# Optimization experiments

Measured on AMD Instinct MI355X. Metric: run time of the kernel, lower is better.

The kernel has to match this reference:

```python
import jax, jax.numpy as jnp
import numpy as np

D_MODEL = 1024
N_HEADS = 16
WINDOW = 64              # window_size
HEAD_DIM = D_MODEL // N_HEADS
HALF = WINDOW // 2
NWIN = WINDOW + 1        # half tokens each side + self
LN_EPS = 1e-5


def _layernorm(x, g, b):
    mu = jnp.mean(x, axis=-1, keepdims=True)
    var = jnp.var(x, axis=-1, keepdims=True)
    return (x - mu) * jax.lax.rsqrt(var + LN_EPS) * g + b


def _linear_attention(q, k, v):
    # feature map phi(x) = elu(x) + 1; O(n) attention over full d_model
    q = jax.nn.elu(q) + 1.0
    k = jax.nn.elu(k) + 1.0
    kv = jnp.einsum('bsd,bse->bde', k, v)          # [B, D, D]
    num = jnp.einsum('bsd,bde->bse', q, kv)        # [B, S, D]
    denom = jnp.einsum('bsd,bd->bs', q, k.sum(axis=1))
    return num / (denom[..., None] + 1e-6)


def _window_attention(q, k, v, rel_bias):
    # sliding window attention with relative position bias, banded via offset scan
    B, S, _ = q.shape
    qh = q.reshape(B, S, N_HEADS, HEAD_DIM).transpose(0, 2, 1, 3)  # [B,H,S,Dh]
    kh = k.reshape(B, S, N_HEADS, HEAD_DIM).transpose(0, 2, 1, 3)
    vh = v.reshape(B, S, N_HEADS, HEAD_DIM).transpose(0, 2, 1, 3)
    kp = jnp.pad(kh, ((0, 0), (0, 0), (HALF, HALF), (0, 0)))
    vp = jnp.pad(vh, ((0, 0), (0, 0), (HALF, HALF), (0, 0)))
    pos = jnp.arange(S)
    scale = np.float32(1.0 / np.sqrt(HEAD_DIM))

    def score_step(_, w):
        off = w - HALF                                   # relative offset in [-HALF, HALF]
        ks = jax.lax.dynamic_slice_in_dim(kp, w, S, axis=2)   # k at position i+off
        s = jnp.einsum('bhsd,bhsd->bhs', qh, ks) * scale
        s = s + rel_bias[off + WINDOW][None, :, None]    # bias per head for this offset
        valid = (pos + off >= 0) & (pos + off < S)
        s = jnp.where(valid[None, None, :], s, -jnp.inf)
        return None, s

    _, scores = jax.lax.scan(score_step, None, jnp.arange(NWIN))  # [W,B,H,S]
    attn = jax.nn.softmax(scores, axis=0)                          # softmax over window

    def out_step(acc, aw):
        a, w = aw
        vs = jax.lax.dynamic_slice_in_dim(vp, w, S, axis=2)
        return acc + a[..., None] * vs, None

    out, _ = jax.lax.scan(out_step, jnp.zeros_like(qh), (attn, jnp.arange(NWIN)))
    return out.transpose(0, 2, 1, 3).reshape(B, S, D_MODEL)


def setup_inputs() -> dict:
    key = jax.random.key(0)
    ks = jax.random.split(key, 16)

    def lin(k, fan_in, shape):
        return (jax.random.normal(k, shape, jnp.float32) / np.sqrt(fan_in)).astype(jnp.float32)

    D = D_MODEL
    inp = {
        'x': jax.random.normal(ks[0], (2, 2048, D), jnp.float32),
        'wq_lin': lin(ks[1], D, (D, D)), 'bq_lin': jnp.zeros((D,), jnp.float32),
        'wk_lin': lin(ks[2], D, (D, D)), 'bk_lin': jnp.zeros((D,), jnp.float32),
        'wv_lin': lin(ks[3], D, (D, D)), 'bv_lin': jnp.zeros((D,), jnp.float32),
        'wq_loc': lin(ks[4], D, (D, D)), 'bq_loc': jnp.zeros((D,), jnp.float32),
        'wk_loc': lin(ks[5], D, (D, D)), 'bk_loc': jnp.zeros((D,), jnp.float32),
        'wv_loc': lin(ks[6], D, (D, D)), 'bv_loc': jnp.zeros((D,), jnp.float32),
        'wo': lin(ks[7], D, (D, D)), 'bo': jnp.zeros((D,), jnp.float32),
        'wg1': lin(ks[8], 3 * D, (3 * D, D)), 'bg1': jnp.zeros((D,), jnp.float32),
        'wg2': lin(ks[9], D, (D, D)), 'bg2': jnp.zeros((D,), jnp.float32),
        'rel_bias': jax.random.normal(ks[10], (2 * WINDOW + 1, N_HEADS), jnp.float32),
        'ln_g': jnp.ones((D,), jnp.float32),
        'ln_b': jnp.zeros((D,), jnp.float32),
    }
    return inp


def reference(x, wq_lin, bq_lin, wk_lin, bk_lin, wv_lin, bv_lin,
              wq_loc, bq_loc, wk_loc, bk_loc, wv_loc, bv_loc,
              wo, bo, wg1, bg1, wg2, bg2, rel_bias, ln_g, ln_b):
    h = _layernorm(x, ln_g, ln_b)
    lin_out = _linear_attention(h @ wq_lin + bq_lin,
                                h @ wk_lin + bk_lin,
                                h @ wv_lin + bv_lin)
    win_out = _window_attention(h @ wq_loc + bq_loc,
                                h @ wk_loc + bk_loc,
                                h @ wv_loc + bv_loc, rel_bias)
    gate_in = jnp.concatenate([lin_out, win_out, h], axis=-1)
    gate = jax.nn.sigmoid(jnp.maximum(gate_in @ wg1 + bg1, 0.0) @ wg2 + bg2)
    out = gate * lin_out + (1.0 - gate) * win_out
    return out @ wo + bo + x
```

## Files before the change

kernel.cpp:

```cpp
#include <hip/hip_runtime.h>

typedef unsigned short u16;
typedef unsigned int u32;
typedef float f32x4 __attribute__((ext_vector_type(4)));
typedef __bf16 bf16x8 __attribute__((ext_vector_type(8)));

#define SEQ 2048
#define DM 1024

__device__ __forceinline__ float bf2f(u16 a){
  u32 b = ((u32)a) << 16; float f; __builtin_memcpy(&f, &b, 4); return f;
}
__device__ __forceinline__ u16 f2bf(float f){
  u32 b; __builtin_memcpy(&b, &f, 4);
  b += 0x7fffu + ((b >> 16) & 1u);
  return (u16)(b >> 16);
}

__device__ __forceinline__ void gload16(const void* g, void* l){
  __builtin_amdgcn_global_load_lds((const __attribute__((address_space(1))) u32*)g,
                                   (__attribute__((address_space(3))) u32*)l, 16, 0, 0);
}

#define SBAR  __builtin_amdgcn_sched_barrier(0); __builtin_amdgcn_s_barrier(); __builtin_amdgcn_sched_barrier(0);
#define VM0   asm volatile("s_waitcnt vmcnt(0)" ::: "memory"); __builtin_amdgcn_sched_barrier(0);
#define VM6   asm volatile("s_waitcnt vmcnt(6)" ::: "memory"); __builtin_amdgcn_sched_barrier(0);
#define VM8   asm volatile("s_waitcnt vmcnt(8)" ::: "memory"); __builtin_amdgcn_sched_barrier(0);

#define MFMA16(AF, BF) \
  __builtin_amdgcn_s_setprio(1); \
  _Pragma("unroll") for (int m_ = 0; m_ < 4; m_++) \
  _Pragma("unroll") for (int n_ = 0; n_ < 4; n_++) \
    acc[m_][n_] = __builtin_amdgcn_mfma_f32_16x16x32_bf16(AF[m_], BF[n_], acc[m_][n_], 0,0,0); \
  __builtin_amdgcn_s_setprio(0);

struct TP { const float* src[9]; u16* dst[9]; int K[9]; };

__global__ __launch_bounds__(256) void ktransall(TP tp){
  __shared__ float tile[64][65];
  int z = blockIdx.z;
  int K = tp.K[z];
  int kb = blockIdx.y << 6, nb = blockIdx.x << 6;
  if (kb >= K) return;
  const float* W = tp.src[z];
  u16* WT = tp.dst[z];
  const int N = 1024;
  int t = threadIdx.x;
  #pragma unroll
  for (int i = 0; i < 4; i++){
    int idx = t + (i << 8);
    int r = idx >> 4, c = (idx & 15) << 2;
    float4 v = *(const float4*)(W + (size_t)(kb + r) * N + nb + c);
    tile[r][c] = v.x; tile[r][c+1] = v.y; tile[r][c+2] = v.z; tile[r][c+3] = v.w;
  }
  __syncthreads();
  #pragma unroll
  for (int i = 0; i < 2; i++){
    int idx = t + (i << 8);
    int n = idx >> 3, k8 = (idx & 7) << 3;
    union { u16 s[8]; int4 v; } u;
    #pragma unroll
    for (int j = 0; j < 8; j++) u.s[j] = f2bf(tile[k8 + j][n]);
    *(int4*)(WT + (size_t)(nb + n) * K + kb + k8) = u.v;
  }
}

__global__ __launch_bounds__(256) void kln(const float* __restrict__ x, const float* __restrict__ gg,
                                           const float* __restrict__ bb, u16* __restrict__ h){
  int row = blockIdx.x, t = threadIdx.x;
  float4 xv = ((const float4*)(x + (size_t)row * DM))[t];
  float s  = xv.x + xv.y + xv.z + xv.w;
  float s2 = xv.x*xv.x + xv.y*xv.y + xv.z*xv.z + xv.w*xv.w;
  #pragma unroll
  for (int o = 1; o < 64; o <<= 1){ s += __shfl_xor(s, o); s2 += __shfl_xor(s2, o); }
  __shared__ float r1[4], r2[4];
  if ((t & 63) == 0){ r1[t >> 6] = s; r2[t >> 6] = s2; }
  __syncthreads();
  float S = r1[0]+r1[1]+r1[2]+r1[3], S2 = r2[0]+r2[1]+r2[2]+r2[3];
  float mu = S * (1.0f/DM);
  float var = S2 * (1.0f/DM) - mu*mu;
  float rstd = rsqrtf(var + 1e-5f);
  float4 gv = ((const float4*)gg)[t], bv = ((const float4*)bb)[t];
  ushort4 o;
  o.x = f2bf((xv.x - mu)*rstd*gv.x + bv.x);
  o.y = f2bf((xv.y - mu)*rstd*gv.y + bv.y);
  o.z = f2bf((xv.z - mu)*rstd*gv.z + bv.z);
  o.w = f2bf((xv.w - mu)*rstd*gv.w + bv.w);
  ((ushort4*)(h + (size_t)row * DM))[t] = o;
}

__device__ __forceinline__ float phi_elu(float v){ return v > 0.f ? v + 1.f : __expf(v); }

__global__ __launch_bounds__(512, 2) void kqkv8(
  const u16* __restrict__ h,
  const u16* wt0, const u16* wt1, const u16* wt2, const u16* wt3, const u16* wt4, const u16* wt5,
  const float* b0, const float* b1, const float* b2, const float* b3, const float* b4, const float* b5,
  u16* phiQ, u16* phiKT, u16* vT, u16* qloc, u16* kloc, u16* vlocT)
{
  extern __shared__ char smem[];
  char* LA0 = smem;
  char* LA1 = smem + 16384;
  char* LB0 = smem + 32768;
  char* LB1 = smem + 65536;

  const int t = threadIdx.x, lane = t & 63, w = t >> 6;
  const int wm = w >> 2, wn = w & 3;

  int bid = blockIdx.x;
  int swz = (bid & 7) * 96 + (bid >> 3);
  int mt = swz & 31, ntile = swz >> 5;
  int m0 = mt << 7;
  int n0g = ntile << 8;
  int wi = n0g >> 10;
  int n0 = n0g & 1023;
  const u16* Bp = wi==0?wt0: wi==1?wt1: wi==2?wt2: wi==3?wt3: wi==4?wt4: wt5;
  const float* bsel = wi==0?b0: wi==1?b1: wi==2?b2: wi==3?b3: wi==4?b4: b5;

  auto stageA = [&](char* dst, int kt){
    #pragma unroll
    for (int j = 0; j < 2; j++){
      int slot = (j << 9) + t;
      int r = slot >> 3;
      int csw = ((slot & 7) << 4) ^ ((r & 7) << 4);
      gload16((const char*)(h + (size_t)(m0 + r) * 1024 + (kt << 6)) + csw,
              dst + (((j << 9) + (w << 6)) << 4));
    }
  };
  auto stageB = [&](char* dst, int kt){
    #pragma unroll
    for (int j = 0; j < 4; j++){
      int slot = (j << 9) + t;
      int r = slot >> 3;
      int csw = ((slot & 7) << 4) ^ ((r & 7) << 4);
      gload16((const char*)(Bp + (size_t)(n0 + r) * 1024 + (kt << 6)) + csw,
              dst + (((j << 9) + (w << 6)) << 4));
    }
  };
  auto rdA = [&](const char* ab, int m, int kk) -> bf16x8 {
    int ra = (wm << 6) + (m << 4) + (lane & 15);
    return *(const bf16x8*)(ab + (ra << 7) + (((kk << 6) + ((lane >> 4) << 4)) ^ ((ra & 7) << 4)));
  };
  auto rdB = [&](const char* bb, int n, int kk) -> bf16x8 {
    int rb = (wn << 6) + (n << 4) + (lane & 15);
    return *(const bf16x8*)(bb + (rb << 7) + (((kk << 6) + ((lane >> 4) << 4)) ^ ((rb & 7) << 4)));
  };

  f32x4 acc[4][4];
  #pragma unroll
  for (int m = 0; m < 4; m++)
    #pragma unroll
    for (int n = 0; n < 4; n++) acc[m][n] = (f32x4){0.f,0.f,0.f,0.f};

  const int NT = 16;
  bf16x8 a0[4], bq0[4], a1[4], bq1[4];

  stageA(LA0, 0); stageB(LB0, 0);
  stageA(LA1, 1); stageB(LB1, 1);
  VM6 SBAR
  #pragma unroll
  for (int m = 0; m < 4; m++) a0[m] = rdA(LA0, m, 0);
  #pragma unroll
  for (int n = 0; n < 4; n++) bq0[n] = rdB(LB0, n, 0);

  #pragma unroll 1
  for (int i = 0; i < NT/2; i++){
    int e = 2*i, o = e + 1;
    int se = (e + 2 < NT) ? e + 2 : NT - 1;
    int so = (o + 2 < NT) ? o + 2 : NT - 1;
    #pragma unroll
    for (int m = 0; m < 4; m++) a1[m] = rdA(LA0, m, 1);
    #pragma unroll
    for (int n = 0; n < 4; n++) bq1[n] = rdB(LB0, n, 1);
    SBAR
    stageA(LA0, se); stageB(LB0, se);
    MFMA16(a0, bq0)
    VM6 SBAR
    #pragma unroll
    for (int m = 0; m < 4; m++) a0[m] = rdA(LA1, m, 0);
    #pragma unroll
    for (int n = 0; n < 4; n++) bq0[n] = rdB(LB1, n, 0);
    MFMA16(a1, bq1)
    #pragma unroll
    for (int m = 0; m < 4; m++) a1[m] = rdA(LA1, m, 1);
    #pragma unroll
    for (int n = 0; n < 4; n++) bq1[n] = rdB(LB1, n, 1);
    SBAR
    stageA(LA1, so); stageB(LB1, so);
    MFMA16(a0, bq0)
    VM6 SBAR
    if (i < NT/2 - 1){
      #pragma unroll
      for (int m = 0; m < 4; m++) a0[m] = rdA(LA0, m, 0);
      #pragma unroll
      for (int n = 0; n < 4; n++) bq0[n] = rdB(LB0, n, 0);
    }
    MFMA16(a1, bq1)
  }
  VM0

  #pragma unroll
  for (int n = 0; n < 4; n++){
    int col = n0 + (wn << 6) + (n << 4) + (lane & 15);
    float bv = bsel[col];
    #pragma unroll
    for (int m = 0; m < 4; m++){
      int r0 = m0 + (wm << 6) + (m << 4) + ((lane >> 4) << 2);
      float e[4];
      #pragma unroll
      for (int r = 0; r < 4; r++) e[r] = acc[m][n][r] + bv;
      if (wi == 0){
        #pragma unroll
        for (int r = 0; r < 4; r++) phiQ[(size_t)(r0 + r) * DM + col] = f2bf(phi_elu(e[r]));
      } else if (wi == 1 || wi == 2 || wi == 5){
        union { u16 s[4]; ushort4 v; } o;
        #pragma unroll
        for (int r = 0; r < 4; r++) o.s[r] = f2bf(wi == 1 ? phi_elu(e[r]) : e[r]);
        int bb = r0 >> 11, sl = r0 & 2047;
        u16* dst = (wi == 1) ? phiKT : (wi == 2 ? vT : vlocT);
        *(ushort4*)(dst + ((size_t)(bb << 10) + col) * SEQ + sl) = o.v;
      } else {
        u16* dst = wi==3 ? qloc : kloc;
        #pragma unroll
        for (int r = 0; r < 4; r++) dst[(size_t)(r0 + r) * DM + col] = f2bf(e[r]);
      }
    }
  }
}

template<int NCHUNK>
__device__ __forceinline__ void pipe128(const u16* A0c, const u16* A1c, const u16* A2c, int lda,
                                        const u16* B, int ldb, int K, int m0, int n0,
                                        char* LA0, char* LA1, char* LB0, char* LB1,
                                        f32x4 (&acc)[4][4])
{
  const int t = threadIdx.x, lane = t & 63, w = t >> 6;
  const int wm = w >> 1, wn = w & 1;
  const int NT = K >> 6;

  auto stageA = [&](char* dst, int kt){
    const u16* Ab;
    if (NCHUNK == 3){
      int ci = kt >> 4;
      const u16* cp = (ci == 0) ? A0c : ((ci == 1) ? A1c : A2c);
      Ab = cp + ((kt & 15) << 6);
    } else {
      Ab = A0c + (kt << 6);
    }
    #pragma unroll
    for (int j = 0; j < 4; j++){
      int slot = (j << 8) + t;
      int r = slot >> 3;
      int csw = ((slot & 7) << 4) ^ ((r & 7) << 4);
      gload16((const char*)(Ab + (size_t)(m0 + r) * lda) + csw,
              dst + (((j << 8) + (w << 6)) << 4));
    }
  };
  auto stageB = [&](char* dst, int kt){
    const u16* Bb = B + (kt << 6);
    #pragma unroll
    for (int j = 0; j < 4; j++){
      int slot = (j << 8) + t;
      int r = slot >> 3;
      int csw = ((slot & 7) << 4) ^ ((r & 7) << 4);
      gload16((const char*)(Bb + (size_t)(n0 + r) * ldb) + csw,
              dst + (((j << 8) + (w << 6)) << 4));
    }
  };
  auto rdA = [&](const char* ab, int m, int kk) -> bf16x8 {
    int ra = (wm << 6) + (m << 4) + (lane & 15);
    return *(const bf16x8*)(ab + (ra << 7) + (((kk << 6) + ((lane >> 4) << 4)) ^ ((ra & 7) << 4)));
  };
  auto rdB = [&](const char* bb, int n, int kk) -> bf16x8 {
    int rb = (wn << 6) + (n << 4) + (lane & 15);
    return *(const bf16x8*)(bb + (rb << 7) + (((kk << 6) + ((lane >> 4) << 4)) ^ ((rb & 7) << 4)));
  };

  bf16x8 a0[4], bq0[4], a1[4], bq1[4];

  stageA(LA0, 0); stageB(LB0, 0);
  stageA(LA1, 1); stageB(LB1, 1);
  VM8 SBAR
  #pragma unroll
  for (int m = 0; m < 4; m++) a0[m] = rdA(LA0, m, 0);
  #pragma unroll
  for (int n = 0; n < 4; n++) bq0[n] = rdB(LB0, n, 0);

  #pragma unroll 1
  for (int i = 0; i < NT/2; i++){
    int e = 2*i, o = e + 1;
    int se = (e + 2 < NT) ? e + 2 : NT - 1;
    int so = (o + 2 < NT) ? o + 2 : NT - 1;
    #pragma unroll
    for (int m = 0; m < 4; m++) a1[m] = rdA(LA0, m, 1);
    #pragma unroll
    for (int n = 0; n < 4; n++) bq1[n] = rdB(LB0, n, 1);
    SBAR
    stageA(LA0, se); stageB(LB0, se);
    MFMA16(a0, bq0)
    VM8 SBAR
    #pragma unroll
    for (int m = 0; m < 4; m++) a0[m] = rdA(LA1, m, 0);
    #pragma unroll
    for (int n = 0; n < 4; n++) bq0[n] = rdB(LB1, n, 0);
    MFMA16(a1, bq1)
    #pragma unroll
    for (int m = 0; m < 4; m++) a1[m] = rdA(LA1, m, 1);
    #pragma unroll
    for (int n = 0; n < 4; n++) bq1[n] = rdB(LB1, n, 1);
    SBAR
    stageA(LA1, so); stageB(LB1, so);
    MFMA16(a0, bq0)
    VM8 SBAR
    if (i < NT/2 - 1){
      #pragma unroll
      for (int m = 0; m < 4; m++) a0[m] = rdA(LA0, m, 0);
      #pragma unroll
      for (int n = 0; n < 4; n++) bq0[n] = rdB(LB0, n, 0);
    }
    MFMA16(a1, bq1)
  }
  VM0
}

#define PIPE_LDS \
  __shared__ char LA0[16384], LA1[16384], LB0[16384], LB1[16384];

#define EPI_COORDS \
  const int lane = threadIdx.x & 63, w = threadIdx.x >> 6; \
  const int wm = w >> 1, wn = w & 1;

#define ZERO_ACC f32x4 acc[4][4]; \
  _Pragma("unroll") for (int m = 0; m < 4; m++) _Pragma("unroll") for (int n = 0; n < 4; n++) acc[m][n] = (f32x4){0.f,0.f,0.f,0.f};

__global__ __launch_bounds__(256) void kkv2(const u16* __restrict__ vT, const u16* __restrict__ phiKT,
                                            u16* __restrict__ kvp0, u16* __restrict__ kvp1){
  PIPE_LDS
  int bid = blockIdx.x;
  int mt = bid & 7, nt = (bid >> 3) & 7, b = (bid >> 6) & 1, kh = bid >> 7;
  int m0 = mt << 7, n0 = nt << 7;
  const u16* A = vT + (size_t)b * DM * SEQ + (kh << 10);
  const u16* B = phiKT + (size_t)b * DM * SEQ + (kh << 10);
  ZERO_ACC
  pipe128<1>(A, 0, 0, SEQ, B, SEQ, 1024, m0, n0, LA0, LA1, LB0, LB1, acc);
  EPI_COORDS
  u16* C = (kh ? kvp1 : kvp0) + (size_t)b * DM * DM;
  #pragma unroll
  for (int n = 0; n < 4; n++){
    int col = n0 + wn*64 + n*16 + (lane & 15);
    #pragma unroll
    for (int m = 0; m < 4; m++){
      int r0 = m0 + wm*64 + m*16 + ((lane >> 4) << 2);
      #pragma unroll
      for (int r = 0; r < 4; r++) C[(size_t)(r0 + r) * DM + col] = f2bf(acc[m][n][r]);
    }
  }
}

__global__ __launch_bounds__(256) void kvadd(const u16* __restrict__ a, const u16* __restrict__ bsrc,
                                             u16* __restrict__ c){
  size_t i = ((size_t)blockIdx.x * 256 + threadIdx.x) * 8;
  int4 ra = *(const int4*)(a + i);
  int4 rb = *(const int4*)(bsrc + i);
  const u16* pa = (const u16*)&ra; const u16* pb = (const u16*)&rb;
  union { u16 s[8]; int4 v; } o;
  #pragma unroll
  for (int j = 0; j < 8; j++) o.s[j] = f2bf(bf2f(pa[j]) + bf2f(pb[j]));
  *(int4*)(c + i) = o.v;
}

__global__ __launch_bounds__(256) void kwinM(
  const u16* __restrict__ qloc, const u16* __restrict__ kloc,
  const u16* __restrict__ vlocT, const float* __restrict__ rel_bias,
  u16* __restrict__ wout)
{
  __shared__ char Qs[8192];
  __shared__ char Ks[16384];
  __shared__ char Vs[16384];
  __shared__ char Ps[16384];
  __shared__ float bias_s[65];

  const int t = threadIdx.x, lane = t & 63, w = t >> 6;
  int bid = blockIdx.x;
  int qt = bid & 31, hh = (bid >> 5) & 15, b = bid >> 9;
  int q0 = qt << 6;
  size_t rowbase = (size_t)b * SEQ;

  #pragma unroll
  for (int j = 0; j < 2; j++){
    int c = (j << 8) + t;
    int row = c >> 3;
    int csw = ((c & 7) << 4) ^ ((row & 7) << 4);
    gload16((const char*)(qloc + (rowbase + q0 + row) * DM + hh*64) + csw,
            Qs + (((j << 8) + (w << 6)) << 4));
  }
  #pragma unroll
  for (int j = 0; j < 4; j++){
    int c = (j << 8) + t;
    int row = c >> 3;
    int csw = ((c & 7) << 4) ^ ((row & 7) << 4);
    int p = q0 + row - 32;
    p = p < 0 ? 0 : (p > SEQ-1 ? SEQ-1 : p);
    gload16((const char*)(kloc + (rowbase + p) * DM + hh*64) + csw,
            Ks + (((j << 8) + (w << 6)) << 4));
  }
  #pragma unroll
  for (int j = 0; j < 4; j++){
    int c = (j << 8) + t;
    int row = c >> 4;
    int csw = ((c & 15) << 4) ^ ((row & 7) << 4);
    int k0 = q0 - 32 + (csw >> 1);
    k0 = k0 < 0 ? 0 : (k0 > SEQ-8 ? SEQ-8 : k0);
    gload16((const char*)(vlocT + ((size_t)(b << 10) + hh*64 + row) * SEQ + k0),
            Vs + (((j << 8) + (w << 6)) << 4));
  }
  if (t < 65) bias_s[t] = rel_bias[(t + 32) * 16 + hh];
  __syncthreads();

  auto rdQ = [&](int kk) -> bf16x8 {
    int ra = (w << 4) + (lane & 15);
    return *(const bf16x8*)(Qs + (ra << 7) + (((kk << 6) + ((lane >> 4) << 4)) ^ ((ra & 7) << 4)));
  };
  auto rdK = [&](int n, int kk) -> bf16x8 {
    int rb = (n << 4) + (lane & 15);
    return *(const bf16x8*)(Ks + (rb << 7) + (((kk << 6) + ((lane >> 4) << 4)) ^ ((rb & 7) << 4)));
  };
  f32x4 sa[8];
  #pragma unroll
  for (int n = 0; n < 8; n++) sa[n] = (f32x4){0.f,0.f,0.f,0.f};
  {
    bf16x8 qf0 = rdQ(0), qf1 = rdQ(1);
    #pragma unroll
    for (int n = 0; n < 8; n++){
      sa[n] = __builtin_amdgcn_mfma_f32_16x16x32_bf16(qf0, rdK(n, 0), sa[n], 0,0,0);
      sa[n] = __builtin_amdgcn_mfma_f32_16x16x32_bf16(qf1, rdK(n, 1), sa[n], 0,0,0);
    }
  }

  int qrel = (w << 4) + ((lane >> 4) << 2);
  float m_[4] = {-1e30f, -1e30f, -1e30f, -1e30f};
  #pragma unroll
  for (int n = 0; n < 8; n++){
    int ridx = (n << 4) + (lane & 15);
    int p = q0 + ridx - 32;
    #pragma unroll
    for (int j = 0; j < 4; j++){
      int d = ridx - (qrel + j);
      bool ok = ((unsigned)d <= 64u) && ((unsigned)p < (unsigned)SEQ);
      float bb = bias_s[(unsigned)d <= 64u ? d : 0];
      float v = ok ? sa[n][j] * 0.125f + bb : -1e30f;
      sa[n][j] = v;
      m_[j] = fmaxf(m_[j], v);
    }
  }
  #pragma unroll
  for (int o = 1; o < 16; o <<= 1){
    #pragma unroll
    for (int j = 0; j < 4; j++) m_[j] = fmaxf(m_[j], __shfl_xor(m_[j], o));
  }
  float l_[4] = {0.f, 0.f, 0.f, 0.f};
  #pragma unroll
  for (int n = 0; n < 8; n++){
    #pragma unroll
    for (int j = 0; j < 4; j++){
      float e = __expf(sa[n][j] - m_[j]);
      sa[n][j] = e;
      l_[j] += e;
    }
  }
  #pragma unroll
  for (int o = 1; o < 16; o <<= 1){
    #pragma unroll
    for (int j = 0; j < 4; j++) l_[j] += __shfl_xor(l_[j], o);
  }

  #pragma unroll
  for (int n = 0; n < 8; n++){
    int colb = ((n << 4) + (lane & 15)) << 1;
    #pragma unroll
    for (int j = 0; j < 4; j++){
      int row = qrel + j;
      *(u16*)(Ps + (row << 8) + (colb ^ ((row & 7) << 4))) = f2bf(sa[n][j]);
    }
  }
  __syncthreads();

  auto rdP = [&](int kk) -> bf16x8 {
    int ra = (w << 4) + (lane & 15);
    return *(const bf16x8*)(Ps + (ra << 8) + (((kk << 6) + ((lane >> 4) << 4)) ^ ((ra & 7) << 4)));
  };
  auto rdV = [&](int n, int kk) -> bf16x8 {
    int rb = (n << 4) + (lane & 15);
    return *(const bf16x8*)(Vs + (rb << 8) + (((kk << 6) + ((lane >> 4) << 4)) ^ ((rb & 7) << 4)));
  };
  f32x4 oa[4];
  #pragma unroll
  for (int n = 0; n < 4; n++) oa[n] = (f32x4){0.f,0.f,0.f,0.f};
  #pragma unroll
  for (int kk = 0; kk < 4; kk++){
    bf16x8 pf = rdP(kk);
    #pragma unroll
    for (int n = 0; n < 4; n++)
      oa[n] = __builtin_amdgcn_mfma_f32_16x16x32_bf16(pf, rdV(n, kk), oa[n], 0,0,0);
  }

  #pragma unroll
  for (int j = 0; j < 4; j++){
    float inv = 1.0f / l_[j];
    int q = q0 + qrel + j;
    u16* dst = wout + (rowbase + q) * DM + hh*64;
    #pragma unroll
    for (int n = 0; n < 4; n++)
      dst[(n << 4) + (lane & 15)] = f2bf(oa[n][j] * inv);
  }
}

__global__ __launch_bounds__(256) void knum(const u16* __restrict__ phiQ, const u16* __restrict__ kvT,
                                            const float* __restrict__ dn, u16* __restrict__ lin){
  PIPE_LDS
  int b = blockIdx.z;
  int m0 = blockIdx.x << 7, n0 = blockIdx.y << 7;
  const u16* A = phiQ + (size_t)b * SEQ * DM;
  const u16* B = kvT + (size_t)b * DM * DM;
  ZERO_ACC
  pipe128<1>(A, 0, 0, DM, B, DM, DM, m0, n0, LA0, LA1, LB0, LB1, acc);
  EPI_COORDS
  #pragma unroll
  for (int n = 0; n < 4; n++){
    int col = n0 + wn*64 + n*16 + (lane & 15);
    #pragma unroll
    for (int m = 0; m < 4; m++){
      int r0 = m0 + wm*64 + m*16 + ((lane >> 4) << 2);
      #pragma unroll
      for (int r = 0; r < 4; r++){
        float d = dn[(b << 11) + r0 + r] + 1e-6f;
        lin[((size_t)(b << 11) + r0 + r) * DM + col] = f2bf(acc[m][n][r] / d);
      }
    }
  }
}

__global__ __launch_bounds__(256) void ksumk(const u16* __restrict__ kt, float* __restrict__ ks){
  int row = blockIdx.x, t = threadIdx.x;
  const ushort4* src = (const ushort4*)(kt + (size_t)row * SEQ);
  float s = 0.f;
  for (int i = t; i < 512; i += 256){
    ushort4 v = src[i];
    s += bf2f(v.x) + bf2f(v.y) + bf2f(v.z) + bf2f(v.w);
  }
  #pragma unroll
  for (int o = 1; o < 64; o <<= 1) s += __shfl_xor(s, o);
  __shared__ float red[4];
  if ((t & 63) == 0) red[t >> 6] = s;
  __syncthreads();
  if (t == 0) ks[row] = red[0] + red[1] + red[2] + red[3];
}

__global__ __launch_bounds__(256) void kdenom(const u16* __restrict__ phiQ, const float* __restrict__ ks,
                                              float* __restrict__ dn){
  int row = blockIdx.x, t = threadIdx.x;
  ushort4 v = ((const ushort4*)(phiQ + (size_t)row * DM))[t];
  float4 kk = ((const float4*)(ks + ((size_t)(row >> 11) << 10)))[t];
  float s = bf2f(v.x)*kk.x + bf2f(v.y)*kk.y + bf2f(v.z)*kk.z + bf2f(v.w)*kk.w;
  #pragma unroll
  for (int o = 1; o < 64; o <<= 1) s += __shfl_xor(s, o);
  __shared__ float red[4];
  if ((t & 63) == 0) red[t >> 6] = s;
  __syncthreads();
  if (t == 0) dn[row] = red[0] + red[1] + red[2] + red[3];
}

__global__ __launch_bounds__(256) void kgate1(const u16* __restrict__ lin, const u16* __restrict__ win,
                                              const u16* __restrict__ h, const u16* __restrict__ wg1T,
                                              const float* __restrict__ bg1, u16* __restrict__ g1){
  PIPE_LDS
  int m0 = blockIdx.x << 7, n0 = blockIdx.y << 7;
  ZERO_ACC
  pipe128<3>(lin, win, h, DM, wg1T, 3072, 3072, m0, n0, LA0, LA1, LB0, LB1, acc);
  EPI_COORDS
  #pragma unroll
  for (int n = 0; n < 4; n++){
    int col = n0 + wn*64 + n*16 + (lane & 15);
    float bv = bg1[col];
    #pragma unroll
    for (int m = 0; m < 4; m++){
      int r0 = m0 + wm*64 + m*16 + ((lane >> 4) << 2);
      #pragma unroll
      for (int r = 0; r < 4; r++){
        float v = acc[m][n][r] + bv;
        g1[(size_t)(r0 + r) * DM + col] = f2bf(v > 0.f ? v : 0.f);
      }
    }
  }
}

__global__ __launch_bounds__(256) void kgate2(const u16* __restrict__ g1, const u16* __restrict__ wg2T,
                                              const float* __restrict__ bg2, const u16* __restrict__ lin,
                                              const u16* __restrict__ win, u16* __restrict__ outc){
  PIPE_LDS
  int m0 = blockIdx.x << 7, n0 = blockIdx.y << 7;
  ZERO_ACC
  pipe128<1>(g1, 0, 0, DM, wg2T, DM, DM, m0, n0, LA0, LA1, LB0, LB1, acc);
  EPI_COORDS
  #pragma unroll
  for (int n = 0; n < 4; n++){
    int col = n0 + wn*64 + n*16 + (lane & 15);
    float bv = bg2[col];
    #pragma unroll
    for (int m = 0; m < 4; m++){
      int r0 = m0 + wm*64 + m*16 + ((lane >> 4) << 2);
      #pragma unroll
      for (int r = 0; r < 4; r++){
        size_t idx = (size_t)(r0 + r) * DM + col;
        float g = 1.0f / (1.0f + __expf(-(acc[m][n][r] + bv)));
        float lv = bf2f(lin[idx]), wv = bf2f(win[idx]);
        outc[idx] = f2bf(g * lv + (1.0f - g) * wv);
      }
    }
  }
}

__global__ __launch_bounds__(256) void kfinal(const u16* __restrict__ outc, const u16* __restrict__ woT,
                                              const float* __restrict__ bo, const float* __restrict__ x,
                                              float* __restrict__ out){
  PIPE_LDS
  int m0 = blockIdx.x << 7, n0 = blockIdx.y << 7;
  ZERO_ACC
  pipe128<1>(outc, 0, 0, DM, woT, DM, DM, m0, n0, LA0, LA1, LB0, LB1, acc);
  EPI_COORDS
  #pragma unroll
  for (int n = 0; n < 4; n++){
    int col = n0 + wn*64 + n*16 + (lane & 15);
    float bv = bo[col];
    #pragma unroll
    for (int m = 0; m < 4; m++){
      int r0 = m0 + wm*64 + m*16 + ((lane >> 4) << 2);
      #pragma unroll
      for (int r = 0; r < 4; r++){
        size_t idx = (size_t)(r0 + r) * DM + col;
        out[idx] = acc[m][n][r] + bv + x[idx];
      }
    }
  }
}

extern "C" void kernel_launch(void* const* d_in, const int* in_sizes, int n_in,
                              void* d_out, int out_size, void* d_ws, size_t ws_size,
                              hipStream_t stream)
{
  const float* x      = (const float*)d_in[0];
  const float* wq_lin = (const float*)d_in[1];  const float* bq_lin = (const float*)d_in[2];
  const float* wk_lin = (const float*)d_in[3];  const float* bk_lin = (const float*)d_in[4];
  const float* wv_lin = (const float*)d_in[5];  const float* bv_lin = (const float*)d_in[6];
  const float* wq_loc = (const float*)d_in[7];  const float* bq_loc = (const float*)d_in[8];
  const float* wk_loc = (const float*)d_in[9];  const float* bk_loc = (const float*)d_in[10];
  const float* wv_loc = (const float*)d_in[11]; const float* bv_loc = (const float*)d_in[12];
  const float* wo     = (const float*)d_in[13]; const float* bo     = (const float*)d_in[14];
  const float* wg1    = (const float*)d_in[15]; const float* bg1    = (const float*)d_in[16];
  const float* wg2    = (const float*)d_in[17]; const float* bg2    = (const float*)d_in[18];
  const float* rel_bias = (const float*)d_in[19];
  const float* ln_g   = (const float*)d_in[20]; const float* ln_b   = (const float*)d_in[21];

  char* ws = (char*)d_ws;
  size_t off = 0;
  auto alloc = [&](size_t bytes) -> void* {
    void* p = ws + off;
    off += (bytes + 255) & ~(size_t)255;
    return p;
  };
  const size_t MB2 = (size_t)1024 * 1024 * 2;
  const size_t ACT = (size_t)4096 * 1024 * 2;
  u16* wT[6]; for (int i = 0; i < 6; i++) wT[i] = (u16*)alloc(MB2);
  u16* woT   = (u16*)alloc(MB2);
  u16* wg1T  = (u16*)alloc((size_t)1024 * 3072 * 2);
  u16* wg2T  = (u16*)alloc(MB2);
  u16* hbf   = (u16*)alloc(ACT);
  u16* phiQ  = (u16*)alloc(ACT);
  u16* phiKT = (u16*)alloc(ACT);
  u16* vT    = (u16*)alloc(ACT);
  u16* qloc  = (u16*)alloc(ACT);
  u16* kloc  = (u16*)alloc(ACT);
  u16* vlocT = (u16*)alloc(ACT);
  u16* kvT   = (u16*)alloc(2 * MB2);
  u16* kvp0  = (u16*)alloc(2 * MB2);
  u16* kvp1  = (u16*)alloc(2 * MB2);
  float* ksum = (float*)alloc(2 * 1024 * 4);
  float* dnm  = (float*)alloc(4096 * 4);
  u16* lin   = (u16*)alloc(ACT);
  u16* win   = (u16*)alloc(ACT);
  u16* g1    = phiQ;
  u16* outc  = vT;

  hipFuncSetAttribute((const void*)kqkv8, hipFuncAttributeMaxDynamicSharedMemorySize, 98304);

  dim3 blk(256);
  TP tp;
  tp.src[0]=wq_lin; tp.src[1]=wk_lin; tp.src[2]=wv_lin; tp.src[3]=wq_loc; tp.src[4]=wk_loc;
  tp.src[5]=wv_loc; tp.src[6]=wo; tp.src[7]=wg1; tp.src[8]=wg2;
  tp.dst[0]=wT[0]; tp.dst[1]=wT[1]; tp.dst[2]=wT[2]; tp.dst[3]=wT[3]; tp.dst[4]=wT[4];
  tp.dst[5]=wT[5]; tp.dst[6]=woT; tp.dst[7]=wg1T; tp.dst[8]=wg2T;
  for (int i = 0; i < 9; i++) tp.K[i] = (i == 7) ? 3072 : 1024;
  ktransall<<<dim3(16,48,9), blk, 0, stream>>>(tp);

  kln<<<4096, blk, 0, stream>>>(x, ln_g, ln_b, hbf);

  kqkv8<<<768, 512, 98304, stream>>>(hbf, wT[0], wT[1], wT[2], wT[3], wT[4], wT[5],
                                     bq_lin, bk_lin, bv_lin, bq_loc, bk_loc, bv_loc,
                                     phiQ, phiKT, vT, qloc, kloc, vlocT);

  ksumk<<<2048, blk, 0, stream>>>(phiKT, ksum);
  kdenom<<<4096, blk, 0, stream>>>(phiQ, ksum, dnm);

  kkv2<<<256, blk, 0, stream>>>(vT, phiKT, kvp0, kvp1);
  kvadd<<<1024, blk, 0, stream>>>(kvp0, kvp1, kvT);

  kwinM<<<1024, blk, 0, stream>>>(qloc, kloc, vlocT, rel_bias, win);

  knum<<<dim3(16,8,2), blk, 0, stream>>>(phiQ, kvT, dnm, lin);

  kgate1<<<dim3(32,8), blk, 0, stream>>>(lin, win, hbf, wg1T, bg1, g1);
  kgate2<<<dim3(32,8), blk, 0, stream>>>(g1, wg2T, bg2, lin, win, outc);
  kfinal<<<dim3(32,8), blk, 0, stream>>>(outc, woT, bo, x, (float*)d_out);
}
```

Before: 227.0 us.

## Rework QKV GEMM to 256-thread 256x128 tiles with triple-buffered K32 stages

The fused six-projection GEMM moves from 512-thread blocks with 128x256 tiles and double-buffered K=64 stages to 256-thread blocks with 256x128 tiles, K=32 stages and a three-deep LDS ring. Each wave now computes a 128x64 sub-tile (8x4 MFMAs), which gives more reuse per fragment, and loads are issued three stages ahead with one barrier per K step. The aim is deeper latency hiding with less LDS (72KB instead of 96KB). The cost is higher register pressure from 32 accumulators and twice as many K iterations, each with a barrier.

```diff
diff --git a/kernel.cpp b/kernel.cpp
--- a/kernel.cpp
+++ b/kernel.cpp
@@ -26,10 +26,18 @@
 #define VM0   asm volatile("s_waitcnt vmcnt(0)" ::: "memory"); __builtin_amdgcn_sched_barrier(0);
 #define VM6   asm volatile("s_waitcnt vmcnt(6)" ::: "memory"); __builtin_amdgcn_sched_barrier(0);
 #define VM8   asm volatile("s_waitcnt vmcnt(8)" ::: "memory"); __builtin_amdgcn_sched_barrier(0);
+#define VM12  asm volatile("s_waitcnt vmcnt(12)" ::: "memory"); __builtin_amdgcn_sched_barrier(0);
 
 #define MFMA16(AF, BF) \
   __builtin_amdgcn_s_setprio(1); \
   _Pragma("unroll") for (int m_ = 0; m_ < 4; m_++) \
+  _Pragma("unroll") for (int n_ = 0; n_ < 4; n_++) \
+    acc[m_][n_] = __builtin_amdgcn_mfma_f32_16x16x32_bf16(AF[m_], BF[n_], acc[m_][n_], 0,0,0); \
+  __builtin_amdgcn_s_setprio(0);
+
+#define MFMA_W(AF, BF) \
+  __builtin_amdgcn_s_setprio(1); \
+  _Pragma("unroll") for (int m_ = 0; m_ < 8; m_++) \
   _Pragma("unroll") for (int n_ = 0; n_ < 4; n_++) \
     acc[m_][n_] = __builtin_amdgcn_mfma_f32_16x16x32_bf16(AF[m_], BF[n_], acc[m_][n_], 0,0,0); \
   __builtin_amdgcn_s_setprio(0);
@@ -91,110 +99,98 @@
 
 __device__ __forceinline__ float phi_elu(float v){ return v > 0.f ? v + 1.f : __expf(v); }
 
-__global__ __launch_bounds__(512, 2) void kqkv8(
+__global__ __launch_bounds__(256, 2) void kqkvW(
   const u16* __restrict__ h,
   const u16* wt0, const u16* wt1, const u16* wt2, const u16* wt3, const u16* wt4, const u16* wt5,
   const float* b0, const float* b1, const float* b2, const float* b3, const float* b4, const float* b5,
   u16* phiQ, u16* phiKT, u16* vT, u16* qloc, u16* kloc, u16* vlocT)
 {
   extern __shared__ char smem[];
-  char* LA0 = smem;
-  char* LA1 = smem + 16384;
-  char* LB0 = smem + 32768;
-  char* LB1 = smem + 65536;
-
   const int t = threadIdx.x, lane = t & 63, w = t >> 6;
-  const int wm = w >> 2, wn = w & 3;
+  const int wm = w >> 1, wn = w & 1;
 
   int bid = blockIdx.x;
   int swz = (bid & 7) * 96 + (bid >> 3);
-  int mt = swz & 31, ntile = swz >> 5;
-  int m0 = mt << 7;
-  int n0g = ntile << 8;
-  int wi = n0g >> 10;
-  int n0 = n0g & 1023;
+  int mt = swz & 15, nt = swz >> 4;
+  int m0 = mt << 8;
+  int wi = nt >> 3;
+  int n0 = (nt & 7) << 7;
   const u16* Bp = wi==0?wt0: wi==1?wt1: wi==2?wt2: wi==3?wt3: wi==4?wt4: wt5;
   const float* bsel = wi==0?b0: wi==1?b1: wi==2?b2: wi==3?b3: wi==4?b4: b5;
 
-  auto stageA = [&](char* dst, int kt){
+  auto stageA = [&](char* buf, int kt){
+    #pragma unroll
+    for (int j = 0; j < 4; j++){
+      int slot = (j << 8) + t;
+      int row = slot >> 2, c = slot & 3;
+      int sc = (c ^ ((row >> 1) & 3)) << 4;
+      gload16((const char*)(h + (size_t)(m0 + row) * 1024 + (kt << 5)) + sc,
+              buf + (((j << 8) + (w << 6)) << 4));
+    }
+  };
+  auto stageB = [&](char* buf, int kt){
     #pragma unroll
     for (int j = 0; j < 2; j++){
-      int slot = (j << 9) + t;
-      int r = slot >> 3;
-      int csw = ((slot & 7) << 4) ^ ((r & 7) << 4);
-      gload16((const char*)(h + (size_t)(m0 + r) * 1024 + (kt << 6)) + csw,
-              dst + (((j << 9) + (w << 6)) << 4));
-    }
-  };
-  auto stageB = [&](char* dst, int kt){
-    #pragma unroll
-    for (int j = 0; j < 4; j++){
-      int slot = (j << 9) + t;
-      int r = slot >> 3;
-      int csw = ((slot & 7) << 4) ^ ((r & 7) << 4);
-      gload16((const char*)(Bp + (size_t)(n0 + r) * 1024 + (kt << 6)) + csw,
-              dst + (((j << 9) + (w << 6)) << 4));
-    }
-  };
-  auto rdA = [&](const char* ab, int m, int kk) -> bf16x8 {
-    int ra = (wm << 6) + (m << 4) + (lane & 15);
-    return *(const bf16x8*)(ab + (ra << 7) + (((kk << 6) + ((lane >> 4) << 4)) ^ ((ra & 7) << 4)));
-  };
-  auto rdB = [&](const char* bb, int n, int kk) -> bf16x8 {
+      int slot = (j << 8) + t;
+      int row = slot >> 2, c = slot & 3;
+      int sc = (c ^ ((row >> 1) & 3)) << 4;
+      gload16((const char*)(Bp + (size_t)(n0 + row) * 1024 + (kt << 5)) + sc,
+              buf + 16384 + (((j << 8) + (w << 6)) << 4));
+    }
+  };
+  auto stage = [&](int bi, int kt){
+    char* buf = smem + bi * 24576;
+    stageA(buf, kt);
+    stageB(buf, kt);
+  };
+  auto rdA = [&](int bi, int m) -> bf16x8 {
+    const char* ab = smem + bi * 24576;
+    int ra = (wm << 7) + (m << 4) + (lane & 15);
+    return *(const bf16x8*)(ab + (ra << 6) + (((lane >> 4) ^ ((ra >> 1) & 3)) << 4));
+  };
+  auto rdB = [&](int bi, int n) -> bf16x8 {
+    const char* bb = smem + bi * 24576 + 16384;
     int rb = (wn << 6) + (n << 4) + (lane & 15);
-    return *(const bf16x8*)(bb + (rb << 7) + (((kk << 6) + ((lane >> 4) << 4)) ^ ((rb & 7) << 4)));
-  };
-
-  f32x4 acc[4][4];
-  #pragma unroll
-  for (int m = 0; m < 4; m++)
+    return *(const bf16x8*)(bb + (rb << 6) + (((lane >> 4) ^ ((rb >> 1) & 3)) << 4));
+  };
+
+  f32x4 acc[8][4];
+  #pragma unroll
+  for (int m = 0; m < 8; m++)
     #pragma unroll
     for (int n = 0; n < 4; n++) acc[m][n] = (f32x4){0.f,0.f,0.f,0.f};
 
-  const int NT = 16;
-  bf16x8 a0[4], bq0[4], a1[4], bq1[4];
-
-  stageA(LA0, 0); stageB(LB0, 0);
-  stageA(LA1, 1); stageB(LB1, 1);
-  VM6 SBAR
-  #pragma unroll
-  for (int m = 0; m < 4; m++) a0[m] = rdA(LA0, m, 0);
-  #pragma unroll
-  for (int n = 0; n < 4; n++) bq0[n] = rdB(LB0, n, 0);
+  const int NT = 32;
+  bf16x8 a0[8], bq0[4], a1[8], bq1[4];
+
+  stage(0, 0); stage(1, 1); stage(2, 2);
+  VM12 SBAR
+  #pragma unroll
+  for (int m = 0; m < 8; m++) a0[m] = rdA(0, m);
+  #pragma unroll
+  for (int n = 0; n < 4; n++) bq0[n] = rdB(0, n);
 
   #pragma unroll 1
   for (int i = 0; i < NT/2; i++){
-    int e = 2*i, o = e + 1;
-    int se = (e + 2 < NT) ? e + 2 : NT - 1;
-    int so = (o + 2 < NT) ? o + 2 : NT - 1;
-    #pragma unroll
-    for (int m = 0; m < 4; m++) a1[m] = rdA(LA0, m, 1);
-    #pragma unroll
-    for (int n = 0; n < 4; n++) bq1[n] = rdB(LB0, n, 1);
-    SBAR
-    stageA(LA0, se); stageB(LB0, se);
-    MFMA16(a0, bq0)
+    int t0 = 2*i, t1 = t0 + 1;
+    int s0 = (t0 + 3 < NT) ? t0 + 3 : NT - 1;
+    int s1 = (t1 + 3 < NT) ? t1 + 3 : NT - 1;
     VM6 SBAR
     #pragma unroll
-    for (int m = 0; m < 4; m++) a0[m] = rdA(LA1, m, 0);
-    #pragma unroll
-    for (int n = 0; n < 4; n++) bq0[n] = rdB(LB1, n, 0);
-    MFMA16(a1, bq1)
-    #pragma unroll
-    for (int m = 0; m < 4; m++) a1[m] = rdA(LA1, m, 1);
-    #pragma unroll
-    for (int n = 0; n < 4; n++) bq1[n] = rdB(LB1, n, 1);
-    SBAR
-    stageA(LA1, so); stageB(LB1, so);
-    MFMA16(a0, bq0)
+    for (int m = 0; m < 8; m++) a1[m] = rdA((t0 + 1) % 3, m);
+    #pragma unroll
+    for (int n = 0; n < 4; n++) bq1[n] = rdB((t0 + 1) % 3, n);
+    stage(t0 % 3, s0);
+    MFMA_W(a0, bq0)
     VM6 SBAR
     if (i < NT/2 - 1){
       #pragma unroll
-      for (int m = 0; m < 4; m++) a0[m] = rdA(LA0, m, 0);
-      #pragma unroll
-      for (int n = 0; n < 4; n++) bq0[n] = rdB(LB0, n, 0);
-    }
-    MFMA16(a1, bq1)
+      for (int m = 0; m < 8; m++) a0[m] = rdA((t1 + 1) % 3, m);
+      #pragma unroll
+      for (int n = 0; n < 4; n++) bq0[n] = rdB((t1 + 1) % 3, n);
+    }
+    stage(t1 % 3, s1);
+    MFMA_W(a1, bq1)
   }
   VM0
 
@@ -203,8 +199,8 @@
     int col = n0 + (wn << 6) + (n << 4) + (lane & 15);
     float bv = bsel[col];
     #pragma unroll
-    for (int m = 0; m < 4; m++){
-      int r0 = m0 + (wm << 6) + (m << 4) + ((lane >> 4) << 2);
+    for (int m = 0; m < 8; m++){
+      int r0 = m0 + (wm << 7) + (m << 4) + ((lane >> 4) << 2);
       float e[4];
       #pragma unroll
       for (int r = 0; r < 4; r++) e[r] = acc[m][n][r] + bv;
@@ -690,7 +686,7 @@
   u16* g1    = phiQ;
   u16* outc  = vT;
 
-  hipFuncSetAttribute((const void*)kqkv8, hipFuncAttributeMaxDynamicSharedMemorySize, 98304);
+  hipFuncSetAttribute((const void*)kqkvW, hipFuncAttributeMaxDynamicSharedMemorySize, 73728);
 
   dim3 blk(256);
   TP tp;
@@ -703,7 +699,7 @@
 
   kln<<<4096, blk, 0, stream>>>(x, ln_g, ln_b, hbf);
 
-  kqkv8<<<768, 512, 98304, stream>>>(hbf, wT[0], wT[1], wT[2], wT[3], wT[4], wT[5],
+  kqkvW<<<768, blk, 73728, stream>>>(hbf, wT[0], wT[1], wT[2], wT[3], wT[4], wT[5],
                                      bq_lin, bk_lin, bv_lin, bq_loc, bk_loc, bv_loc,
                                      phiQ, phiKT, vT, qloc, kloc, vlocT);
 
```

Result: no change. 224.9 us (-0.9%).

## Merge KV GEMM and window attention into one heterogeneous-block kernel launch

Applied to the files above, without the earlier changes.

Combines the split-K kv GEMM kernel and the window-attention kernel into a single launch of 1280 blocks. The first 256 blocks run the GEMM and the rest run window attention, sharing one dynamic LDS buffer. The aim is to fill the GPU with the 256-block GEMM plus the attention blocks at the same time, cutting idle compute units and a launch boundary. In exchange, every block now reserves 64KB of LDS, which may lower occupancy for the attention blocks, and both paths share one register allocation.

```diff
diff --git a/kernel.cpp b/kernel.cpp
--- a/kernel.cpp
+++ b/kernel.cpp
@@ -332,56 +332,45 @@
 #define ZERO_ACC f32x4 acc[4][4]; \
   _Pragma("unroll") for (int m = 0; m < 4; m++) _Pragma("unroll") for (int n = 0; n < 4; n++) acc[m][n] = (f32x4){0.f,0.f,0.f,0.f};
 
-__global__ __launch_bounds__(256) void kkv2(const u16* __restrict__ vT, const u16* __restrict__ phiKT,
-                                            u16* __restrict__ kvp0, u16* __restrict__ kvp1){
-  PIPE_LDS
-  int bid = blockIdx.x;
-  int mt = bid & 7, nt = (bid >> 3) & 7, b = (bid >> 6) & 1, kh = bid >> 7;
-  int m0 = mt << 7, n0 = nt << 7;
-  const u16* A = vT + (size_t)b * DM * SEQ + (kh << 10);
-  const u16* B = phiKT + (size_t)b * DM * SEQ + (kh << 10);
-  ZERO_ACC
-  pipe128<1>(A, 0, 0, SEQ, B, SEQ, 1024, m0, n0, LA0, LA1, LB0, LB1, acc);
-  EPI_COORDS
-  u16* C = (kh ? kvp1 : kvp0) + (size_t)b * DM * DM;
-  #pragma unroll
-  for (int n = 0; n < 4; n++){
-    int col = n0 + wn*64 + n*16 + (lane & 15);
-    #pragma unroll
-    for (int m = 0; m < 4; m++){
-      int r0 = m0 + wm*64 + m*16 + ((lane >> 4) << 2);
-      #pragma unroll
-      for (int r = 0; r < 4; r++) C[(size_t)(r0 + r) * DM + col] = f2bf(acc[m][n][r]);
-    }
-  }
-}
-
-__global__ __launch_bounds__(256) void kvadd(const u16* __restrict__ a, const u16* __restrict__ bsrc,
-                                             u16* __restrict__ c){
-  size_t i = ((size_t)blockIdx.x * 256 + threadIdx.x) * 8;
-  int4 ra = *(const int4*)(a + i);
-  int4 rb = *(const int4*)(bsrc + i);
-  const u16* pa = (const u16*)&ra; const u16* pb = (const u16*)&rb;
-  union { u16 s[8]; int4 v; } o;
-  #pragma unroll
-  for (int j = 0; j < 8; j++) o.s[j] = f2bf(bf2f(pa[j]) + bf2f(pb[j]));
-  *(int4*)(c + i) = o.v;
-}
-
-__global__ __launch_bounds__(256) void kwinM(
+__global__ __launch_bounds__(256) void kkvw(
+  const u16* __restrict__ vT, const u16* __restrict__ phiKT,
+  u16* __restrict__ kvp0, u16* __restrict__ kvp1,
   const u16* __restrict__ qloc, const u16* __restrict__ kloc,
   const u16* __restrict__ vlocT, const float* __restrict__ rel_bias,
   u16* __restrict__ wout)
 {
-  __shared__ char Qs[8192];
-  __shared__ char Ks[16384];
-  __shared__ char Vs[16384];
-  __shared__ char Ps[16384];
-  __shared__ float bias_s[65];
-
+  extern __shared__ char sm[];
   const int t = threadIdx.x, lane = t & 63, w = t >> 6;
   int bid = blockIdx.x;
-  int qt = bid & 31, hh = (bid >> 5) & 15, b = bid >> 9;
+  if (bid < 256){
+    int mt = bid & 7, nt = (bid >> 3) & 7, b = (bid >> 6) & 1, kh = bid >> 7;
+    int m0 = mt << 7, n0 = nt << 7;
+    const u16* A = vT + (size_t)b * DM * SEQ + (kh << 10);
+    const u16* B = phiKT + (size_t)b * DM * SEQ + (kh << 10);
+    char* LA0 = sm; char* LA1 = sm + 16384; char* LB0 = sm + 32768; char* LB1 = sm + 49152;
+    ZERO_ACC
+    pipe128<1>(A, 0, 0, SEQ, B, SEQ, 1024, m0, n0, LA0, LA1, LB0, LB1, acc);
+    const int wm = w >> 1, wn = w & 1;
+    u16* C = (kh ? kvp1 : kvp0) + (size_t)b * DM * DM;
+    #pragma unroll
+    for (int n = 0; n < 4; n++){
+      int col = n0 + wn*64 + n*16 + (lane & 15);
+      #pragma unroll
+      for (int m = 0; m < 4; m++){
+        int r0 = m0 + wm*64 + m*16 + ((lane >> 4) << 2);
+        #pragma unroll
+        for (int r = 0; r < 4; r++) C[(size_t)(r0 + r) * DM + col] = f2bf(acc[m][n][r]);
+      }
+    }
+    return;
+  }
+  char* Qs = sm;
+  char* Ks = sm + 8192;
+  char* Vs = sm + 24576;
+  char* Ps = sm + 40960;
+  float* bias_s = (float*)(sm + 57344);
+  int i = bid - 256;
+  int qt = i & 31, hh = (i >> 5) & 15, b = i >> 9;
   int q0 = qt << 6;
   size_t rowbase = (size_t)b * SEQ;
 
@@ -512,6 +501,18 @@
     for (int n = 0; n < 4; n++)
       dst[(n << 4) + (lane & 15)] = f2bf(oa[n][j] * inv);
   }
+}
+
+__global__ __launch_bounds__(256) void kvadd(const u16* __restrict__ a, const u16* __restrict__ bsrc,
+                                             u16* __restrict__ c){
+  size_t i = ((size_t)blockIdx.x * 256 + threadIdx.x) * 8;
+  int4 ra = *(const int4*)(a + i);
+  int4 rb = *(const int4*)(bsrc + i);
+  const u16* pa = (const u16*)&ra; const u16* pb = (const u16*)&rb;
+  union { u16 s[8]; int4 v; } o;
+  #pragma unroll
+  for (int j = 0; j < 8; j++) o.s[j] = f2bf(bf2f(pa[j]) + bf2f(pb[j]));
+  *(int4*)(c + i) = o.v;
 }
 
 __global__ __launch_bounds__(256) void knum(const u16* __restrict__ phiQ, const u16* __restrict__ kvT,
@@ -691,6 +692,7 @@
   u16* outc  = vT;
 
   hipFuncSetAttribute((const void*)kqkv8, hipFuncAttributeMaxDynamicSharedMemorySize, 98304);
+  hipFuncSetAttribute((const void*)kkvw, hipFuncAttributeMaxDynamicSharedMemorySize, 65536);
 
   dim3 blk(256);
   TP tp;
@@ -707,13 +709,11 @@
                                      bq_lin, bk_lin, bv_lin, bq_loc, bk_loc, bv_loc,
                                      phiQ, phiKT, vT, qloc, kloc, vlocT);
 
+  kkvw<<<1280, blk, 65536, stream>>>(vT, phiKT, kvp0, kvp1, qloc, kloc, vlocT, rel_bias, win);
+
   ksumk<<<2048, blk, 0, stream>>>(phiKT, ksum);
   kdenom<<<4096, blk, 0, stream>>>(phiQ, ksum, dnm);
-
-  kkv2<<<256, blk, 0, stream>>>(vT, phiKT, kvp0, kvp1);
   kvadd<<<1024, blk, 0, stream>>>(kvp0, kvp1, kvT);
-
-  kwinM<<<1024, blk, 0, stream>>>(qloc, kloc, vlocT, rel_bias, win);
 
   knum<<<dim3(16,8,2), blk, 0, stream>>>(phiQ, kvT, dnm, lin);
 
```

After: 219.0 us. -3.5%, faster.
